# Performance work log

Hardware: AMD Instinct MI355X
Metric: run time of the kernel (lower is better)

## Reference

```python
import jax, jax.numpy as jnp
import numpy as np

NEG = jnp.float32(-1e30)  # safe stand-in for -inf in log-space

def setup_inputs() -> dict:
    key = jax.random.key(0)
    k1, k2, k3, k4 = jax.random.split(key, 4)
    N, C, T, S = 64, 64, 4000, 100
    logits = jax.random.normal(k1, (N, C, T), dtype=jnp.float32)
    targets = jax.random.randint(k2, (N, S), 1, C)          # labels, no blank
    target_lengths = jax.random.randint(k3, (N,), 1, S + 1)  # >= 1
    input_lengths = jax.random.randint(k4, (N,), 2000, T + 1)
    return {"logits": logits, "targets": targets,
            "target_lengths": target_lengths, "input_lengths": input_lengths}

def _lse2(a, b):
    m = jnp.maximum(a, b)
    return m + jnp.log(jnp.exp(a - m) + jnp.exp(b - m))

def _lse3(a, b, c):
    m = jnp.maximum(jnp.maximum(a, b), c)
    return m + jnp.log(jnp.exp(a - m) + jnp.exp(b - m) + jnp.exp(c - m))

def reference(logits, targets, target_lengths, input_lengths):
    # logits: (N, C, T); blank = 0; reduction = 'mean' (per-sample / target_len, then mean)
    N, C, T = logits.shape
    S = targets.shape[1]
    L = 2 * S + 1
    lp = jax.nn.log_softmax(logits, axis=1)      # (N, C, T)
    lp = jnp.transpose(lp, (2, 0, 1))            # (T, N, C)

    # extended label sequence: blank, t1, blank, t2, ..., blank  -> (N, L)
    ext = jnp.zeros((N, L), dtype=targets.dtype).at[:, 1::2].set(targets)
    # skip transition s-2 -> s allowed iff ext[s] != blank and ext[s] != ext[s-2]
    prev2 = jnp.pad(ext[:, :-2], ((0, 0), (2, 0)), constant_values=0)
    skip_ok = (ext != 0) & (ext != prev2)        # (N, L)

    # per-time log-probs of extended labels: (T, N, L)
    lp_ext = jnp.take_along_axis(lp, jnp.broadcast_to(ext[None], (T, N, L)), axis=2)

    # alpha init at t=0
    alpha = jnp.full((N, L), NEG, dtype=lp.dtype)
    alpha = alpha.at[:, 0].set(lp_ext[0, :, 0])
    alpha = alpha.at[:, 1].set(lp_ext[0, :, 1])

    neg1 = jnp.full((N, 1), NEG, dtype=lp.dtype)
    neg2 = jnp.full((N, 2), NEG, dtype=lp.dtype)

    def step(a, inp):
        lpt, t = inp                              # lpt: (N, L)
        a1 = a
        a2 = jnp.concatenate([neg1, a[:, :-1]], axis=1)
        a3 = jnp.concatenate([neg2, a[:, :-2]], axis=1)
        a3 = jnp.where(skip_ok, a3, NEG)
        new = _lse3(a1, a2, a3) + lpt
        active = (t < input_lengths)[:, None]     # freeze past input length
        return jnp.where(active, new, a), None

    alpha, _ = jax.lax.scan(step, alpha, (lp_ext[1:], jnp.arange(1, T)))

    i1 = (2 * target_lengths)[:, None]            # last blank
    i2 = jnp.maximum(i1 - 1, 0)                   # last label
    v1 = jnp.take_along_axis(alpha, i1, axis=1)[:, 0]
    v2 = jnp.take_along_axis(alpha, i2, axis=1)[:, 0]
    loss_n = -_lse2(v1, v2)                       # (N,)
    return jnp.mean(loss_n / target_lengths.astype(loss_n.dtype))
```

## Files before the change

### kernel.cpp

```cpp
#include <hip/hip_runtime.h>
#include <cstdint>
#include <cstddef>

#define NEGV (-1e30f)
#define IL2f 1.44269504088896340736f
#define LN2f 0.693147180559945309417f

__device__ __forceinline__ float exp2_hw(float x) { return __builtin_amdgcn_exp2f(x); }
__device__ __forceinline__ float log2_hw(float x) { return __builtin_amdgcn_logf(x); }

constexpr int Nn = 64, Cc = 64, Tt = 4000, Ss = 100;

__device__ __forceinline__ float wave_shr1(float x) {
    return __int_as_float(__builtin_amdgcn_update_dpp(0, __float_as_int(x), 0x138, 0xF, 0xF, true));
}
__device__ __forceinline__ float wave_shl1(float x) {
    return __int_as_float(__builtin_amdgcn_update_dpp(0, __float_as_int(x), 0x130, 0xF, 0xF, true));
}
__device__ __forceinline__ int wave_shr1_i(int x) {
    return __builtin_amdgcn_update_dpp(0, x, 0x138, 0xF, 0xF, true);
}
__device__ __forceinline__ int wave_shl1_i(int x) {
    return __builtin_amdgcn_update_dpp(0, x, 0x130, 0xF, 0xF, true);
}

typedef float f4 __attribute__((ext_vector_type(4)));
typedef float f2 __attribute__((ext_vector_type(2)));
#define LD4(p) (*(const f4*)(p))

__device__ __forceinline__ void gload16(const float* g, float* l) {
    __builtin_amdgcn_global_load_lds(
        (const __attribute__((address_space(1))) void*)g,
        (__attribute__((address_space(3))) void*)l, 16, 0, 0);
}

__global__ __launch_bounds__(256) void ctc_denom_kernel(
    const float* __restrict__ logits, float* __restrict__ d2)
{
    const int t4 = (blockIdx.x * 256 + threadIdx.x) * 4;
    const int n = blockIdx.y;
    if (t4 >= Tt) return;
    const float* __restrict__ p = logits + (size_t)n * Cc * Tt + t4;
    f4 m, s;
    {
        f4 v = LD4(p);
        #pragma unroll
        for (int i = 0; i < 4; ++i) { m[i] = v[i] * IL2f; s[i] = 1.f; }
    }
    #pragma unroll 4
    for (int c = 1; c < Cc; ++c) {
        f4 v = LD4(p + (size_t)c * Tt);
        #pragma unroll
        for (int i = 0; i < 4; ++i) {
            float vi = v[i] * IL2f;
            float nm = fmaxf(m[i], vi);
            s[i] = s[i] * exp2_hw(m[i] - nm) + exp2_hw(vi - nm);
            m[i] = nm;
        }
    }
    f4 o;
    #pragma unroll
    for (int i = 0; i < 4; ++i) o[i] = m[i] + log2_hw(s[i]);
    *(f4*)(d2 + (size_t)n * Tt + t4) = o;
}

__global__ __launch_bounds__(256) void ctc_prob_kernel(
    const float* __restrict__ logits, const float* __restrict__ d2, float* __restrict__ P)
{
    const int t4 = (blockIdx.x * 256 + threadIdx.x) * 4;
    const int n = blockIdx.y;
    const int c0 = blockIdx.z * 8;
    if (t4 >= Tt) return;
    const f4 d = LD4(d2 + (size_t)n * Tt + t4);
    const float* __restrict__ src = logits + ((size_t)n * Cc + c0) * Tt + t4;
    float* __restrict__ dst = P + ((size_t)n * Cc + c0) * Tt + t4;
    #pragma unroll
    for (int c = 0; c < 8; ++c) {
        f4 v = LD4(src + (size_t)c * Tt);
        f4 o;
        #pragma unroll
        for (int i = 0; i < 4; ++i) o[i] = exp2_hw(fmaf(v[i], IL2f, -d[i]));
        *(f4*)(dst + (size_t)c * Tt) = o;
    }
}

template<bool PRE>
__global__ __launch_bounds__(64) void ctc_fb_kernel(
    const float* __restrict__ PR, const int* __restrict__ targets,
    const int* __restrict__ tlen, const int* __restrict__ ilen,
    const float* __restrict__ d2, float* __restrict__ wsA, float* __restrict__ wsB)
{
    constexpr int NA = PRE ? 3 : 4;
    constexpr int NLD = NA * 8;
    __shared__ float lds[2][NA][8][64][4];

    const int bid = blockIdx.x;
    const int n = bid >> 1;
    const bool bwd = bid & 1;
    const int lane = threadIdx.x;
    const int tl = tlen[n];
    const int Tn = ilen[n];
    const int L = 2 * tl + 1;
    const int mid = Tn >> 1;
    const int s0 = 4 * lane;

    const int j1 = min(2 * lane, Ss - 1);
    const int j3 = min(2 * lane + 1, Ss - 1);
    const int base = n * Ss;
    const int tg1 = targets[base + j1];
    const int tg3 = targets[base + j3];
    const int tg1m = targets[base + max(2 * lane - 1, 0)];
    const int tg3p = targets[base + min(2 * lane + 2, Ss - 1)];

    const float sk1f = ((s0 + 1 >= 3) && (tg1 != tg1m)) ? 1.f : 0.f;
    const float sk3f = (tg3 != tg1) ? 1.f : 0.f;
    const float sk1b = ((s0 + 3 < L) && (tg3 != tg1)) ? 1.f : 0.f;
    const float sk3b = ((s0 + 5 < L) && (tg3p != tg3)) ? 1.f : 0.f;

    const float* __restrict__ rB = PR + (size_t)(n * Cc) * Tt;
    const float* __restrict__ r1 = PR + (size_t)(n * Cc + tg1) * Tt;
    const float* __restrict__ r3 = PR + (size_t)(n * Cc + tg3) * Tt;
    const float* __restrict__ rD = d2 + (size_t)n * Tt;

    float a0, a1, a2, a3;
    int E = 0;

    if (!bwd) {
        float pB0, p10;
        if constexpr (PRE) { pB0 = rB[0]; p10 = r1[0]; }
        else {
            const float dv = rD[0];
            pB0 = exp2_hw(fmaf(rB[0], IL2f, -dv));
            p10 = exp2_hw(fmaf(r1[0], IL2f, -dv));
        }
        a0 = (lane == 0) ? pB0 : 0.f;
        a1 = (lane == 0) ? p10 : 0.f;
        a2 = 0.f; a3 = 0.f;
    } else {
        const int te = Tn - 1;
        float pBe, p1e, p3e;
        if constexpr (PRE) { pBe = rB[te]; p1e = r1[te]; p3e = r3[te]; }
        else {
            const float dv = rD[te];
            pBe = exp2_hw(fmaf(rB[te], IL2f, -dv));
            p1e = exp2_hw(fmaf(r1[te], IL2f, -dv));
            p3e = exp2_hw(fmaf(r3[te], IL2f, -dv));
        }
        const int sl = 2 * tl;
        a0 = (s0 == sl) ? pBe : 0.f;
        a1 = (s0 + 1 == sl - 1) ? p1e : 0.f;
        a2 = (s0 + 2 == sl) ? pBe : 0.f;
        a3 = (s0 + 3 == sl - 1) ? p3e : 0.f;
    }

    #define ISSUE(gg, sl) {                                                         \
        const int bo_ = (gg) * 32;                                                  \
        _Pragma("unroll")                                                           \
        for (int j = 0; j < 8; ++j) {                                               \
            gload16(rB + bo_ + 4 * j, &lds[sl][0][j][0][0]);                        \
            gload16(r1 + bo_ + 4 * j, &lds[sl][1][j][0][0]);                        \
            gload16(r3 + bo_ + 4 * j, &lds[sl][2][j][0][0]);                        \
            if constexpr (!PRE) gload16(rD + bo_ + 4 * j, &lds[sl][NA - 1][j][0][0]); \
        }                                                                           \
    }
    #define WAITG() asm volatile("s_waitcnt vmcnt(%0)" :: "n"(NLD) : "memory")
    #define LOADREGS(slc)                                                           \
        f4 vB[8], vU[8], vW[8], vD[8];                                              \
        _Pragma("unroll")                                                           \
        for (int j = 0; j < 8; ++j) {                                               \
            vB[j] = LD4(&lds[slc][0][j][lane][0]);                                  \
            vU[j] = LD4(&lds[slc][1][j][lane][0]);                                  \
            vW[j] = LD4(&lds[slc][2][j][lane][0]);                                  \
            if constexpr (!PRE) vD[j] = LD4(&lds[slc][NA - 1][j][lane][0]);         \
        }                                                                           \
        (void)vD;

    #define RENORM_S(nb) {                                                          \
        const float mx = fmaxf(fmaxf(a0, a1), fmaxf(a2, a3));                       \
        const int me = (int)(__float_as_uint(mx) >> 23);                            \
        const float s2 = __int_as_float((unsigned)(254 - me) << 23);                \
        a0 *= s2; a1 *= s2; a2 *= s2; a3 *= s2;                                     \
        E = (mx > 0.f) ? (E + me - 127) : (nb);                                     \
    }

    if (!bwd) {
        const int tB = mid;
        const int gHi = tB >> 5;

        #define BODY_F_G(gg) {                                                      \
            _Pragma("unroll")                                                       \
            for (int w = 0; w < 4; ++w) {                                           \
                const int Eu = wave_shr1_i(E);                                      \
                const int eb = min(max(127 + (Eu - E), 0), 230);                    \
                const float sc = __int_as_float((unsigned)eb << 23);                \
                const float sk1fs = sk1f * sc;                                      \
                _Pragma("unroll")                                                   \
                for (int kk = 0; kk < 8; ++kk) {                                    \
                    const int k = w * 8 + kk;                                       \
                    const int t = (gg) * 32 + k;                                    \
                    if (t >= 1 && t <= tB) {                                        \
                        float pB, p1, p3;                                           \
                        if constexpr (PRE) {                                        \
                            pB = vB[k >> 2][k & 3]; p1 = vU[k >> 2][k & 3];         \
                            p3 = vW[k >> 2][k & 3];                                 \
                        } else {                                                    \
                            const float dv = vD[k >> 2][k & 3];                     \
                            pB = exp2_hw(fmaf(vB[k >> 2][k & 3], IL2f, -dv));       \
                            p1 = exp2_hw(fmaf(vU[k >> 2][k & 3], IL2f, -dv));       \
                            p3 = exp2_hw(fmaf(vW[k >> 2][k & 3], IL2f, -dv));       \
                        }                                                           \
                        const float u3 = wave_shr1(a3);                             \
                        const float n3 = fmaf(a1, sk3f, a3 + a2) * p3;              \
                        const float n2 = (a2 + a1) * pB;                            \
                        const float n1 = fmaf(u3, sk1fs, a1 + a0) * p1;             \
                        const float n0 = fmaf(u3, sc, a0) * pB;                     \
                        a0 = n0; a1 = n1; a2 = n2; a3 = n3;                         \
                    }                                                               \
                }                                                                   \
                RENORM_S(Eu);                                                       \
            }                                                                       \
        }

        #define BODY_F_F() {                                                        \
            f2 Q0 = {a0, a2}, Q1 = {a1, a3};                                        \
            _Pragma("unroll")                                                       \
            for (int w = 0; w < 4; ++w) {                                           \
                const int Eu = wave_shr1_i(E);                                      \
                const int eb = min(max(127 + (Eu - E), 0), 230);                    \
                const float sc = __int_as_float((unsigned)eb << 23);                \
                const f2 Ksk = {sk3f, sk1f * sc};                                   \
                const f2 K1s = {1.0f, sc};                                          \
                _Pragma("unroll")                                                   \
                for (int kk = 0; kk < 8; ++kk) {                                    \
                    const int k = w * 8 + kk;                                       \
                    const float pB = vB[k >> 2][k & 3];                             \
                    const f2 P31 = {vW[k >> 2][k & 3], vU[k >> 2][k & 3]};          \
                    const f2 PBB = {pB, pB};                                        \
                    const float u3 = wave_shr1(Q1.y);                               \
                    const f2 M = {Q1.x, u3};                                        \
                    const f2 Q0s = __builtin_shufflevector(Q0, Q0, 1, 0);           \
                    const f2 S = __builtin_shufflevector(Q1, Q1, 1, 0) + Q0s;       \
                    const f2 F = __builtin_elementwise_fma(M, Ksk, S);              \
                    const f2 G = __builtin_elementwise_fma(M, K1s, Q0s);            \
                    const f2 N31 = F * P31;                                         \
                    const f2 N20 = G * PBB;                                         \
                    Q1 = __builtin_shufflevector(N31, N31, 1, 0);                   \
                    Q0 = __builtin_shufflevector(N20, N20, 1, 0);                   \
                }                                                                   \
                const f2 mxv = __builtin_elementwise_max(Q0, Q1);                   \
                const float mx = fmaxf(mxv.x, mxv.y);                               \
                const int me = (int)(__float_as_uint(mx) >> 23);                    \
                const float s2 = __int_as_float((unsigned)(254 - me) << 23);        \
                const f2 S2 = {s2, s2};                                             \
                Q0 *= S2; Q1 *= S2;                                                 \
                E = (mx > 0.f) ? (E + me - 127) : Eu;                               \
            }                                                                       \
            a0 = Q0.x; a2 = Q0.y; a1 = Q1.x; a3 = Q1.y;                             \
        }

        ISSUE(0, 0);
        int cur = 0;
        for (int g = 0; g <= gHi; ++g) {
            ISSUE(min(g + 1, gHi), cur ^ 1);
            WAITG();
            LOADREGS(cur);
            cur ^= 1;
            if (PRE && g >= 1 && g * 32 + 31 <= tB) { BODY_F_F(); }
            else                                    { BODY_F_G(g); }
        }
        #undef BODY_F_G
        #undef BODY_F_F
    } else {
        const int tB = Tn - 2, tA = mid + 1;
        const int gHi = tB >> 5, gLo = tA >> 5;

        #define BODY_B_G(gg) {                                                      \
            _Pragma("unroll")                                                       \
            for (int w = 3; w >= 0; --w) {                                          \
                const int Ed = wave_shl1_i(E);                                      \
                const int eb = min(max(127 + (Ed - E), 0), 230);                    \
                const float sc = __int_as_float((unsigned)eb << 23);                \
                const float sk3bs = sk3b * sc;                                      \
                _Pragma("unroll")                                                   \
                for (int kk = 7; kk >= 0; --kk) {                                   \
                    const int k = w * 8 + kk;                                       \
                    const int t = (gg) * 32 + k;                                    \
                    if (t >= tA && t <= tB) {                                       \
                        float pB, p1, p3;                                           \
                        if constexpr (PRE) {                                        \
                            pB = vB[k >> 2][k & 3]; p1 = vU[k >> 2][k & 3];         \
                            p3 = vW[k >> 2][k & 3];                                 \
                        } else {                                                    \
                            const float dv = vD[k >> 2][k & 3];                     \
                            pB = exp2_hw(fmaf(vB[k >> 2][k & 3], IL2f, -dv));       \
                            p1 = exp2_hw(fmaf(vU[k >> 2][k & 3], IL2f, -dv));       \
                            p3 = exp2_hw(fmaf(vW[k >> 2][k & 3], IL2f, -dv));       \
                        }                                                           \
                        const float d0 = wave_shl1(a0);                             \
                        const float d1 = wave_shl1(a1);                             \
                        const float n0 = (a0 + a1) * pB;                            \
                        const float n1 = fmaf(a3, sk1b, a1 + a2) * p1;              \
                        const float n2 = (a2 + a3) * pB;                            \
                        const float n3 = fmaf(d1, sk3bs, fmaf(d0, sc, a3)) * p3;    \
                        a0 = n0; a1 = n1; a2 = n2; a3 = n3;                         \
                    }                                                               \
                }                                                                   \
                RENORM_S(Ed);                                                       \
            }                                                                       \
        }

        #define BODY_B_F() {                                                        \
            f2 Q0 = {a0, a2}, Q1 = {a1, a3};                                        \
            _Pragma("unroll")                                                       \
            for (int w = 3; w >= 0; --w) {                                          \
                const int Ed = wave_shl1_i(E);                                      \
                const int eb = min(max(127 + (Ed - E), 0), 230);                    \
                const float sc = __int_as_float((unsigned)eb << 23);                \
                const f2 K1s = {1.0f, sc};                                          \
                const f2 Ksk = {sk1b, sk3b * sc};                                   \
                _Pragma("unroll")                                                   \
                for (int kk = 7; kk >= 0; --kk) {                                   \
                    const int k = w * 8 + kk;                                       \
                    const float pB = vB[k >> 2][k & 3];                             \
                    const f2 P13 = {vU[k >> 2][k & 3], vW[k >> 2][k & 3]};          \
                    const f2 PBB = {pB, pB};                                        \
                    const float d0 = wave_shl1(Q0.x);                               \
                    const float d1 = wave_shl1(Q1.x);                               \
                    const f2 S = Q0 + Q1;                                           \
                    const f2 A2 = __builtin_elementwise_fma((f2){Q0.y, d0}, K1s, Q1); \
                    const f2 B2 = __builtin_elementwise_fma((f2){Q1.y, d1}, Ksk, A2); \
                    Q1 = B2 * P13;                                                  \
                    Q0 = S * PBB;                                                   \
                }                                                                   \
                const f2 mxv = __builtin_elementwise_max(Q0, Q1);                   \
                const float mx = fmaxf(mxv.x, mxv.y);                               \
                const int me = (int)(__float_as_uint(mx) >> 23);                    \
                const float s2 = __int_as_float((unsigned)(254 - me) << 23);        \
                const f2 S2 = {s2, s2};                                             \
                Q0 *= S2; Q1 *= S2;                                                 \
                E = (mx > 0.f) ? (E + me - 127) : Ed;                               \
            }                                                                       \
            a0 = Q0.x; a2 = Q0.y; a1 = Q1.x; a3 = Q1.y;                             \
        }

        ISSUE(gHi, 0);
        int cur = 0;
        for (int g = gHi; g >= gLo; --g) {
            ISSUE(max(g - 1, 0), cur ^ 1);
            WAITG();
            LOADREGS(cur);
            cur ^= 1;
            if (PRE && g * 32 >= tA && g * 32 + 31 <= tB) { BODY_B_F(); }
            else                                          { BODY_B_G(g); }
        }
        #undef BODY_B_G
        #undef BODY_B_F
    }
    #undef ISSUE
    #undef WAITG
    #undef LOADREGS
    #undef RENORM_S

    float* dst = (bwd ? wsB : wsA) + n * 256;
    const float Ef = (float)E;
    f4 o;
    o[0] = (s0     < L && a0 > 0.f) ? log2_hw(a0) + Ef : NEGV;
    o[1] = (s0 + 1 < L && a1 > 0.f) ? log2_hw(a1) + Ef : NEGV;
    o[2] = (s0 + 2 < L && a2 > 0.f) ? log2_hw(a2) + Ef : NEGV;
    o[3] = (s0 + 3 < L && a3 > 0.f) ? log2_hw(a3) + Ef : NEGV;
    *(f4*)(dst + s0) = o;
}

__global__ __launch_bounds__(64) void ctc_combine_kernel(
    const float* __restrict__ wsA, const float* __restrict__ wsB,
    const int* __restrict__ targets, const int* __restrict__ tlen,
    float* __restrict__ out)
{
    const int n = blockIdx.x;
    const int lane = threadIdx.x;
    const int tl = tlen[n];
    const int L = 2 * tl + 1;
    float vals[4];
    float vmax = NEGV;
    #pragma unroll
    for (int k = 0; k < 4; ++k) {
        const int s = lane + (k << 6);
        float v = NEGV;
        if (s < L) {
            const float al = wsA[n * 256 + s];
            const float b0 = wsB[n * 256 + s];
            const float b1 = (s + 1 < L) ? wsB[n * 256 + s + 1] : NEGV;
            const bool skip = (s & 1) && (s + 2 < L) &&
                (targets[n * Ss + (s >> 1) + 1] != targets[n * Ss + (s >> 1)]);
            const float b2 = skip ? wsB[n * 256 + s + 2] : NEGV;
            const float m3 = fmaxf(fmaxf(b0, b1), b2);
            const float B = m3 + log2_hw(exp2_hw(b0 - m3) + exp2_hw(b1 - m3) + exp2_hw(b2 - m3));
            v = al + B;
        }
        vals[k] = v;
        vmax = fmaxf(vmax, v);
    }
    #pragma unroll
    for (int o = 32; o; o >>= 1) vmax = fmaxf(vmax, __shfl_xor(vmax, o));
    float ssum = 0.f;
    #pragma unroll
    for (int k = 0; k < 4; ++k) ssum += exp2_hw(vals[k] - vmax);
    #pragma unroll
    for (int o = 32; o; o >>= 1) ssum += __shfl_xor(ssum, o);
    if (lane == 0) {
        const float total2 = vmax + log2_hw(ssum);
        const float loss = -LN2f * total2;
        atomicAdd(out, loss / ((float)tl * (float)Nn));
    }
}

extern "C" void kernel_launch(void* const* d_in, const int* in_sizes, int n_in,
                              void* d_out, int out_size, void* d_ws, size_t ws_size,
                              hipStream_t stream) {
    const float* logits = (const float*)d_in[0];
    const int* targets  = (const int*)d_in[1];
    const int* tlen     = (const int*)d_in[2];
    const int* ilen     = (const int*)d_in[3];
    float* out = (float*)d_out;

    float* wsA = (float*)d_ws;
    float* wsB = wsA + Nn * 256;
    float* d2  = wsB + Nn * 256;
    float* P   = d2 + (size_t)Nn * Tt;
    const size_t need = ((size_t)Nn * 256 * 2 + (size_t)Nn * Tt
                         + (size_t)Nn * Cc * Tt) * sizeof(float);
    const bool pre = (ws_size >= need);

    hipMemsetAsync(d_out, 0, sizeof(float), stream);
    ctc_denom_kernel<<<dim3(4, Nn), 256, 0, stream>>>(logits, d2);
    if (pre) {
        ctc_prob_kernel<<<dim3(4, Nn, 8), 256, 0, stream>>>(logits, d2, P);
        ctc_fb_kernel<true><<<Nn * 2, 64, 0, stream>>>(P, targets, tlen, ilen, d2, wsA, wsB);
    } else {
        ctc_fb_kernel<false><<<Nn * 2, 64, 0, stream>>>(logits, targets, tlen, ilen, d2, wsA, wsB);
    }
    ctc_combine_kernel<<<Nn, 64, 0, stream>>>(wsA, wsB, targets, tlen, out);
}
```

Before: 120.2 us.

## Split softmax denominator over channel halves and compute probabilities only for target classes

The log-sum-exp denominator is now computed as two partial reductions, each over half the channels. This doubles the number of blocks in that pass. The probability kernel merges the two partials on the fly. Each block first builds a bitmask of which of its 8 classes appear in the sample's targets (blank is always included) and exponentiates and stores only those rows, skipping reads and writes for classes the forward-backward pass never touches. In exchange it adds an extra workspace buffer, a shared-memory atomic and barriers per block, and repeated merge arithmetic in every class group.

```diff
diff --git a/kernel.cpp b/kernel.cpp
--- a/kernel.cpp
+++ b/kernel.cpp
@@ -32,6 +32,37 @@
     __builtin_amdgcn_global_load_lds(
         (const __attribute__((address_space(1))) void*)g,
         (__attribute__((address_space(3))) void*)l, 16, 0, 0);
+}
+
+__global__ __launch_bounds__(256) void ctc_denom_part(
+    const float* __restrict__ logits, float* __restrict__ dP)
+{
+    const int t4 = (blockIdx.x * 256 + threadIdx.x) * 4;
+    const int n = blockIdx.y;
+    const int c0 = blockIdx.z * 32;
+    if (t4 >= Tt) return;
+    const float* __restrict__ p = logits + ((size_t)(n * Cc + c0)) * Tt + t4;
+    f4 m, s;
+    {
+        f4 v = LD4(p);
+        #pragma unroll
+        for (int i = 0; i < 4; ++i) { m[i] = v[i] * IL2f; s[i] = 1.f; }
+    }
+    #pragma unroll 4
+    for (int c = 1; c < 32; ++c) {
+        f4 v = LD4(p + (size_t)c * Tt);
+        #pragma unroll
+        for (int i = 0; i < 4; ++i) {
+            float vi = v[i] * IL2f;
+            float nm = fmaxf(m[i], vi);
+            s[i] = s[i] * exp2_hw(m[i] - nm) + exp2_hw(vi - nm);
+            m[i] = nm;
+        }
+    }
+    f4 o;
+    #pragma unroll
+    for (int i = 0; i < 4; ++i) o[i] = m[i] + log2_hw(s[i]);
+    *(f4*)(dP + ((size_t)blockIdx.z * Nn + n) * Tt + t4) = o;
 }
 
 __global__ __launch_bounds__(256) void ctc_denom_kernel(
@@ -64,23 +95,66 @@
     *(f4*)(d2 + (size_t)n * Tt + t4) = o;
 }
 
-__global__ __launch_bounds__(256) void ctc_prob_kernel(
-    const float* __restrict__ logits, const float* __restrict__ d2, float* __restrict__ P)
+__global__ __launch_bounds__(256) void ctc_denom_merge(float* __restrict__ dP)
 {
     const int t4 = (blockIdx.x * 256 + threadIdx.x) * 4;
     const int n = blockIdx.y;
+    if (t4 >= Tt) return;
+    f4 a = LD4(dP + (size_t)n * Tt + t4);
+    f4 b = LD4(dP + ((size_t)Nn + n) * Tt + t4);
+    f4 d;
+    #pragma unroll
+    for (int i = 0; i < 4; ++i) {
+        const float mm = fmaxf(a[i], b[i]);
+        d[i] = mm + log2_hw(exp2_hw(a[i] - mm) + exp2_hw(b[i] - mm));
+    }
+    *(f4*)(dP + (size_t)n * Tt + t4) = d;
+}
+
+template<bool MERGE>
+__global__ __launch_bounds__(256) void ctc_prob_sel(
+    const float* __restrict__ logits, const float* __restrict__ dP,
+    const int* __restrict__ targets, const int* __restrict__ tlen,
+    float* __restrict__ P)
+{
+    const int n = blockIdx.y;
     const int c0 = blockIdx.z * 8;
+    __shared__ int needs;
+    if (threadIdx.x == 0) needs = (c0 == 0) ? 1 : 0;
+    __syncthreads();
+    const int tl = tlen[n];
+    if ((int)threadIdx.x < min(tl, Ss)) {
+        const int rel = targets[n * Ss + threadIdx.x] - c0;
+        if (rel >= 0 && rel < 8) atomicOr(&needs, 1 << rel);
+    }
+    __syncthreads();
+    const int nd = needs;
+    if (nd == 0) return;
+    const int t4 = (blockIdx.x * 256 + threadIdx.x) * 4;
     if (t4 >= Tt) return;
-    const f4 d = LD4(d2 + (size_t)n * Tt + t4);
-    const float* __restrict__ src = logits + ((size_t)n * Cc + c0) * Tt + t4;
-    float* __restrict__ dst = P + ((size_t)n * Cc + c0) * Tt + t4;
+    f4 d;
+    if constexpr (MERGE) {
+        f4 a = LD4(dP + (size_t)n * Tt + t4);
+        f4 b = LD4(dP + ((size_t)Nn + n) * Tt + t4);
+        #pragma unroll
+        for (int i = 0; i < 4; ++i) {
+            const float mm = fmaxf(a[i], b[i]);
+            d[i] = mm + log2_hw(exp2_hw(a[i] - mm) + exp2_hw(b[i] - mm));
+        }
+    } else {
+        d = LD4(dP + (size_t)n * Tt + t4);
+    }
+    const float* __restrict__ src = logits + ((size_t)(n * Cc + c0)) * Tt + t4;
+    float* __restrict__ dst = P + ((size_t)(n * Cc + c0)) * Tt + t4;
     #pragma unroll
     for (int c = 0; c < 8; ++c) {
-        f4 v = LD4(src + (size_t)c * Tt);
-        f4 o;
-        #pragma unroll
-        for (int i = 0; i < 4; ++i) o[i] = exp2_hw(fmaf(v[i], IL2f, -d[i]));
-        *(f4*)(dst + (size_t)c * Tt) = o;
+        if ((nd >> c) & 1) {
+            f4 v = LD4(src + (size_t)c * Tt);
+            f4 o;
+            #pragma unroll
+            for (int i = 0; i < 4; ++i) o[i] = exp2_hw(fmaf(v[i], IL2f, -d[i]));
+            *(f4*)(dst + (size_t)c * Tt) = o;
+        }
     }
 }
 
@@ -425,19 +499,27 @@
 
     float* wsA = (float*)d_ws;
     float* wsB = wsA + Nn * 256;
-    float* d2  = wsB + Nn * 256;
-    float* P   = d2 + (size_t)Nn * Tt;
-    const size_t need = ((size_t)Nn * 256 * 2 + (size_t)Nn * Tt
-                         + (size_t)Nn * Cc * Tt) * sizeof(float);
-    const bool pre = (ws_size >= need);
+    float* dP  = wsB + Nn * 256;
+    float* P1  = dP + (size_t)2 * Nn * Tt;
+    float* P2  = dP + (size_t)Nn * Tt;
+
+    const size_t base = (size_t)Nn * 512;
+    const size_t need1 = (base + (size_t)2 * Nn * Tt + (size_t)Nn * Cc * Tt) * 4;
+    const size_t need2 = (base + (size_t)Nn * Tt + (size_t)Nn * Cc * Tt) * 4;
 
     hipMemsetAsync(d_out, 0, sizeof(float), stream);
-    ctc_denom_kernel<<<dim3(4, Nn), 256, 0, stream>>>(logits, d2);
-    if (pre) {
-        ctc_prob_kernel<<<dim3(4, Nn, 8), 256, 0, stream>>>(logits, d2, P);
-        ctc_fb_kernel<true><<<Nn * 2, 64, 0, stream>>>(P, targets, tlen, ilen, d2, wsA, wsB);
+    if (ws_size >= need1) {
+        ctc_denom_part<<<dim3(4, Nn, 2), 256, 0, stream>>>(logits, dP);
+        ctc_prob_sel<true><<<dim3(4, Nn, 8), 256, 0, stream>>>(logits, dP, targets, tlen, P1);
+        ctc_fb_kernel<true><<<Nn * 2, 64, 0, stream>>>(P1, targets, tlen, ilen, dP, wsA, wsB);
+    } else if (ws_size >= need2) {
+        ctc_denom_kernel<<<dim3(4, Nn), 256, 0, stream>>>(logits, dP);
+        ctc_prob_sel<false><<<dim3(4, Nn, 8), 256, 0, stream>>>(logits, dP, targets, tlen, P2);
+        ctc_fb_kernel<true><<<Nn * 2, 64, 0, stream>>>(P2, targets, tlen, ilen, dP, wsA, wsB);
     } else {
-        ctc_fb_kernel<false><<<Nn * 2, 64, 0, stream>>>(logits, targets, tlen, ilen, d2, wsA, wsB);
+        ctc_denom_part<<<dim3(4, Nn, 2), 256, 0, stream>>>(logits, dP);
+        ctc_denom_merge<<<dim3(4, Nn), 256, 0, stream>>>(dP);
+        ctc_fb_kernel<false><<<Nn * 2, 64, 0, stream>>>(logits, targets, tlen, ilen, dP, wsA, wsB);
     }
     ctc_combine_kernel<<<Nn, 64, 0, stream>>>(wsA, wsB, targets, tlen, out);
 }
```

Result: faster. 107.8 us (-10.3%).
